# Kernel optimization log

Measured on AMD Instinct MI355X. Metric: run time of the kernel, lower is better.

## Reference

```python
import jax, jax.numpy as jnp
import numpy as np

N, M, B = 2048, 2048, 1
D, H, DQK, DV = 1024, 16, 64, 64
OFFSET = 0
PARAM_SCALE = 0.02  # keeps logits in a sane range (original uses plain randn)


def setup_inputs() -> dict:
    key = jax.random.key(0)
    ks = jax.random.split(key, 7)
    return {
        "x_q": jax.random.normal(ks[0], (N, B, D), jnp.float32),
        "x_kv": jax.random.normal(ks[1], (M, B, D), jnp.float32),
        "to_q": jax.random.normal(ks[2], (DQK, H, D), jnp.float32) * PARAM_SCALE,
        "to_k": jax.random.normal(ks[3], (DQK, H, D), jnp.float32) * PARAM_SCALE,
        "to_v": jax.random.normal(ks[4], (DV, H, D), jnp.float32) * PARAM_SCALE,
        "to_out": jax.random.normal(ks[5], (D, DV, H), jnp.float32) * PARAM_SCALE,
        "for_pos_enc": jax.random.normal(ks[6], (DQK, H, D), jnp.float32) * PARAM_SCALE,
    }


def _sincos(n, m, offset, d_x_kv, dtype):
    # relative distances i - j + offset range over [offset-(m-1), offset+(n-1)]
    r = jnp.arange(offset - (m - 1), offset + (n - 1) + 1, dtype=dtype)  # [R], R=n+m-1
    inv_freq = 1.0 / (10000.0 ** (jnp.arange(0.0, d_x_kv, 2.0, dtype=dtype) / d_x_kv))
    phases = r[:, None] * inv_freq[None, :]  # [R, d/2]
    return jnp.concatenate([jnp.sin(phases), jnp.cos(phases)], axis=-1)  # [R, d]


def reference(x_q, x_kv, to_q, to_k, to_v, to_out, for_pos_enc):
    n, b, _ = x_q.shape
    m = x_kv.shape[0]
    # q: [n, d_qk, b, h]
    q = jnp.einsum('dhb,nab->ndah', to_q, x_q)
    # content logits: [n, m, b, h]
    k = jnp.einsum('dhc,mac->mdah', to_k, x_kv)
    content = jnp.einsum('ndah,mdah->nmah', q, k)
    # relative positional encoding (same math as pos_enc[dists - min] then einsum,
    # but logits computed per relative position then gathered -> no [n,m,d,h] blowup)
    sincos = _sincos(n, m, OFFSET, x_kv.shape[-1], x_q.dtype)  # [R, d_x_kv]
    pe_rel = jnp.einsum('dhb,rb->rdh', for_pos_enc, sincos)    # [R, d_qk, h]
    pl_rel = jnp.einsum('ndah,rdh->nrah', q, pe_rel)            # [n, R, b, h]
    idx = jnp.arange(n)[:, None] - jnp.arange(m)[None, :] + (m - 1)  # dists - dists.min()
    position = pl_rel[jnp.arange(n)[:, None], idx]               # [n, m, b, h]
    logits = content + position
    # causal mask: True above diagonal shifted by 1+offset
    mask = jnp.triu(jnp.ones((n, m), bool), 1 + OFFSET)
    logits = jnp.where(mask[:, :, None, None], -jnp.inf, logits)
    weights = jax.nn.softmax(logits, axis=1)                     # softmax over m
    v = jnp.einsum('chb,mab->mach', to_v, x_kv)                  # [m, b, dv, h]
    ctx = jnp.einsum('nmah,mach->nach', weights, v)              # [n, b, dv, h]
    out = jnp.einsum('dch,nach->nad', to_out, ctx)               # [n, b, d]
    return out
```

## Files before the change

kernel.cpp:

```cpp
#include <hip/hip_runtime.h>
#include <hip/hip_bf16.h>

#define N_Q   2048
#define M_KV  2048
#define DIM   1024
#define NH    16
#define DHEAD 64
#define KDIM  1024
#define PEROWS 2112
#define PEBUF  2176

typedef __attribute__((ext_vector_type(8))) __bf16 bf16x8;
typedef __attribute__((ext_vector_type(4))) float  f32x4;

typedef __attribute__((address_space(1))) const unsigned char gbyte_t;
typedef __attribute__((address_space(3))) unsigned char lbyte_t;

__device__ __forceinline__ unsigned short f2bf(float f) {
  union { float f; unsigned u; } v; v.f = f;
  unsigned u = v.u;
  u = u + 0x7fffu + ((u >> 16) & 1u);
  return (unsigned short)(u >> 16);
}

__global__ void cvt2_bf16_kernel(const float* __restrict__ xq, const float* __restrict__ xkv,
                                 unsigned short* __restrict__ oq, unsigned short* __restrict__ okv) {
  int e = blockIdx.x * 256 + threadIdx.x;
  if (e < N_Q * DIM) oq[e] = f2bf(xq[e]);
  else               okv[e - N_Q * DIM] = f2bf(xkv[e - N_Q * DIM]);
}

__global__ void pack4_kernel(const float* __restrict__ wq, const float* __restrict__ wk,
                             const float* __restrict__ wv, const float* __restrict__ wp,
                             unsigned short* __restrict__ oq, unsigned short* __restrict__ okv,
                             unsigned short* __restrict__ op) {
  int gid = blockIdx.x * 256 + threadIdx.x;
  int which = gid >> 20;
  int e = gid & ((1 << 20) - 1);
  int j = e >> 10, b = e & 1023;
  int d = j & 63, h = j >> 6;
  const float* w = (which == 0) ? wq : (which == 1) ? wk : (which == 2) ? wv : wp;
  unsigned short* o = (which == 0) ? oq : (which == 1) ? okv : (which == 2) ? (okv + (size_t)DIM * DIM) : op;
  o[e] = f2bf(w[(d * NH + h) * DIM + b]);
}

__global__ void pack_wo_kernel(const float* __restrict__ w,
                               unsigned short* __restrict__ out) {
  int e = blockIdx.x * 256 + threadIdx.x;
  int dd = e >> 10, j = e & 1023;
  int c = j & 63, h = j >> 6;
  out[e] = f2bf(w[(dd * DHEAD + c) * NH + h]);
}

__global__ void sincos_kernel(unsigned short* __restrict__ out) {
  int e = blockIdx.x * 256 + threadIdx.x;
  int r = e >> 10, i = e & 1023;
  int k2 = (i < 512) ? i : (i - 512);
  float ex = (float)(2 * k2) * (1.0f / 1024.0f);
  float invf = __expf(-ex * 9.210340371976184f);
  float ph = (float)(r - 63) * invf;
  out[e] = f2bf((i < 512) ? __sinf(ph) : __cosf(ph));
}

template<int MODE>
__global__ __launch_bounds__(256) void gemm128_kernel(
    const unsigned short* __restrict__ A, const unsigned short* __restrict__ B,
    void* __restrict__ C1, void* __restrict__ C2, int Mr, int maxBrow) {
  __shared__ unsigned short As[2][128][64];
  __shared__ unsigned short Bs[2][64][64];
  int tid  = threadIdx.x;
  int wave = tid >> 6, lane = tid & 63;
  int g = lane >> 4, r16 = lane & 15;
  int arow0 = blockIdx.x * 128;
  int brow0 = blockIdx.y * 64;
  int amax  = Mr - 1;

  auto stage = [&](int buf, int kt) {
    #pragma unroll
    for (int n = 0; n < 4; ++n) {
      int seg  = wave * 4 + n;
      int rloc = seg * 8 + (lane >> 3);
      int cbyte = ((lane & 7) << 4) ^ ((rloc & 7) << 4);
      int grow = min(arow0 + rloc, amax);
      const unsigned short* gp = A + (size_t)grow * KDIM + kt + (cbyte >> 1);
      __builtin_amdgcn_global_load_lds((gbyte_t*)(const void*)gp,
                                       (lbyte_t*)(void*)&As[buf][seg * 8][0], 16, 0, 0);
    }
    #pragma unroll
    for (int n = 0; n < 2; ++n) {
      int seg  = wave * 2 + n;
      int rloc = seg * 8 + (lane >> 3);
      int cbyte = ((lane & 7) << 4) ^ ((rloc & 7) << 4);
      int grow = min(brow0 + rloc, maxBrow);
      const unsigned short* gp = B + (size_t)grow * KDIM + kt + (cbyte >> 1);
      __builtin_amdgcn_global_load_lds((gbyte_t*)(const void*)gp,
                                       (lbyte_t*)(void*)&Bs[buf][seg * 8][0], 16, 0, 0);
    }
  };

  f32x4 acc[2][4];
  #pragma unroll
  for (int i = 0; i < 2; ++i)
    #pragma unroll
    for (int j = 0; j < 4; ++j) acc[i][j] = (f32x4){0,0,0,0};

  stage(0, 0);
  asm volatile("s_waitcnt vmcnt(0)" ::: "memory");
  __syncthreads();

  int buf = 0;
  for (int t = 0; t < 16; ++t) {
    if (t < 15) stage(buf ^ 1, (t + 1) * 64);

    bf16x8 af[2][2], bf[4][2];
    #pragma unroll
    for (int i = 0; i < 2; ++i)
      #pragma unroll
      for (int kk = 0; kk < 2; ++kk) {
        int r = wave * 32 + i * 16 + r16;
        int cb = ((kk << 6) | (g << 4)) ^ ((r & 7) << 4);
        af[i][kk] = *(const bf16x8*)((const char*)&As[buf][r][0] + cb);
      }
    #pragma unroll
    for (int j = 0; j < 4; ++j)
      #pragma unroll
      for (int kk = 0; kk < 2; ++kk) {
        int r = j * 16 + r16;
        int cb = ((kk << 6) | (g << 4)) ^ ((r & 7) << 4);
        bf[j][kk] = *(const bf16x8*)((const char*)&Bs[buf][r][0] + cb);
      }
    #pragma unroll
    for (int kk = 0; kk < 2; ++kk)
      #pragma unroll
      for (int i = 0; i < 2; ++i)
        #pragma unroll
        for (int j = 0; j < 4; ++j)
          acc[i][j] = __builtin_amdgcn_mfma_f32_16x16x32_bf16(af[i][kk], bf[j][kk], acc[i][j], 0, 0, 0);

    if (t < 15) {
      asm volatile("s_waitcnt vmcnt(0)" ::: "memory");
      __syncthreads();
      buf ^= 1;
    }
  }

  #pragma unroll
  for (int i = 0; i < 2; ++i)
    #pragma unroll
    for (int j = 0; j < 4; ++j)
      #pragma unroll
      for (int rr = 0; rr < 4; ++rr) {
        int row = arow0 + wave * 32 + i * 16 + g * 4 + rr;
        int col = brow0 + j * 16 + r16;
        float v = acc[i][j][rr];
        if (MODE == 0) {
          if (row < Mr) ((float*)C1)[(size_t)row * 1024 + col] = v;
        } else if (MODE == 1) {
          if (row < Mr) ((unsigned short*)C1)[(size_t)row * 1024 + col] = f2bf(v);
        } else {
          if (col < 1024) ((unsigned short*)C1)[(size_t)row * 1024 + col] = f2bf(v);
          else            ((unsigned short*)C2)[(size_t)(col - 1024) * M_KV + row] = f2bf(v);
        }
      }
}

__global__ __launch_bounds__(256, 2) void attn_mfma_kernel(
    const unsigned short* __restrict__ qb, const unsigned short* __restrict__ kb,
    const unsigned short* __restrict__ vt, const unsigned short* __restrict__ pe,
    unsigned short* __restrict__ ctx, float* __restrict__ part) {
  int ord  = (int)blockIdx.x;
  int h    = ord & 15;
  int widx = 79 - (ord >> 4);
  int b, c;
  if (widx < 8)       { b = widx;                                  c = 0; }
  else if (widx < 24) { int t2 = widx - 8;  b = 8  + (t2 >> 1);    c = t2 & 1; }
  else if (widx < 48) { int t2 = widx - 24; int q3 = t2 / 3; b = 16 + q3; c = t2 - 3 * q3; }
  else                { int t2 = widx - 48; b = 24 + (t2 >> 2);    c = t2 & 3; }
  int n0   = b * 64;
  int nc   = (b < 8) ? 1 : (b >> 3) + 1;
  int t0   = c * 8;
  int tend = min(t0 + 8, b + 1);

  int wave = threadIdx.x >> 6;
  int lane = threadIdx.x & 63;
  int g    = lane >> 4;
  int r16  = lane & 15;

  __shared__ unsigned short Ks[2][64][64];
  __shared__ unsigned short Vs[2][64][64];
  __shared__ unsigned short PEs[2][128][64];
  __shared__ unsigned short W_lds[4][16][72];

  const unsigned short* qrow = qb + (size_t)(n0 + wave * 16 + r16) * DIM + h * 64 + g * 8;
  bf16x8 aq0 = *(const bf16x8*)(qrow);
  bf16x8 aq1 = *(const bf16x8*)(qrow + 32);

  union { unsigned short u[8]; bf16x8 v; } one_u;
  #pragma unroll
  for (int i = 0; i < 8; ++i) one_u.u[i] = 0x3F80;
  bf16x8 ones = one_u.v;

  f32x4 acc[4] = {{0,0,0,0},{0,0,0,0},{0,0,0,0},{0,0,0,0}};
  f32x4 lacc = {0,0,0,0};

  auto stage = [&](int bufn, int tilen) {
    int m0n = tilen * 64;
    int prb = n0 - m0n;
    #pragma unroll
    for (int n = 0; n < 2; ++n) {
      int seg  = wave * 2 + n;
      int rloc = seg * 8 + (lane >> 3);
      int cbyte = ((lane & 7) << 4) ^ ((rloc & 7) << 4);
      const unsigned short* gpk = kb + (size_t)(m0n + rloc) * KDIM + h * 64 + (cbyte >> 1);
      __builtin_amdgcn_global_load_lds((gbyte_t*)(const void*)gpk,
                                       (lbyte_t*)(void*)&Ks[bufn][seg * 8][0], 16, 0, 0);
      const unsigned short* gpv = vt + (size_t)(h * 64 + rloc) * M_KV + m0n + (cbyte >> 1);
      __builtin_amdgcn_global_load_lds((gbyte_t*)(const void*)gpv,
                                       (lbyte_t*)(void*)&Vs[bufn][seg * 8][0], 16, 0, 0);
    }
    #pragma unroll
    for (int n = 0; n < 4; ++n) {
      int seg  = wave * 4 + n;
      int rloc = seg * 8 + (lane >> 3);
      int cbyte = ((lane & 7) << 4) ^ ((rloc & 7) << 4);
      const unsigned short* gpp = pe + (size_t)(prb + rloc) * KDIM + h * 64 + (cbyte >> 1);
      __builtin_amdgcn_global_load_lds((gbyte_t*)(const void*)gpp,
                                       (lbyte_t*)(void*)&PEs[bufn][seg * 8][0], 16, 0, 0);
    }
  };

  int srcl[4]; bool hi_sel[4];
  #pragma unroll
  for (int rr = 0; rr < 4; ++rr) {
    srcl[rr]   = (g << 4) | ((g * 4 + rr + 63 - r16) & 15);
    hi_sel[rr] = (g * 4 + rr) > r16;
  }
  int sw = (r16 & 7) << 4;

  stage(0, t0);
  asm volatile("s_waitcnt vmcnt(0)" ::: "memory");
  __syncthreads();

  int buf = 0;
  for (int tile = t0; tile < tend; ++tile) {
    int m0 = tile * 64;
    if (tile + 1 < tend) stage(buf ^ 1, tile + 1);

    f32x4 s[4];
    #pragma unroll
    for (int ct = 0; ct < 4; ++ct) {
      const char* kbase = (const char*)&Ks[buf][ct * 16 + r16][0];
      bf16x8 k0 = *(const bf16x8*)(kbase + (((g << 4)) ^ sw));
      bf16x8 k1 = *(const bf16x8*)(kbase + ((64 | (g << 4)) ^ sw));
      f32x4 z = {0,0,0,0};
      z = __builtin_amdgcn_mfma_f32_16x16x32_bf16(aq0, k0, z, 0, 0, 0);
      z = __builtin_amdgcn_mfma_f32_16x16x32_bf16(aq1, k1, z, 0, 0, 0);
      s[ct] = z;
    }

    f32x4 z2[5];
    #pragma unroll
    for (int cp = 0; cp < 5; ++cp) {
      const char* pbase = (const char*)&PEs[buf][wave * 16 + cp * 16 + r16][0];
      bf16x8 p0 = *(const bf16x8*)(pbase + (((g << 4)) ^ sw));
      bf16x8 p1 = *(const bf16x8*)(pbase + ((64 | (g << 4)) ^ sw));
      f32x4 z = {0,0,0,0};
      z = __builtin_amdgcn_mfma_f32_16x16x32_bf16(aq0, p0, z, 0, 0, 0);
      z = __builtin_amdgcn_mfma_f32_16x16x32_bf16(aq1, p1, z, 0, 0, 0);
      z2[cp] = z;
    }

    bool diag = (m0 == n0);
    #pragma unroll
    for (int ct = 0; ct < 4; ++ct) {
      #pragma unroll
      for (int rr = 0; rr < 4; ++rr) {
        float vhi = __shfl(z2[4 - ct][rr], srcl[rr], 64);
        float vlo = __shfl(z2[3 - ct][rr], srcl[rr], 64);
        float p   = hi_sel[rr] ? vhi : vlo;
        int il = g * 4 + rr;
        int it = wave * 16 + il;
        int jt = ct * 16 + r16;
        float val = s[ct][rr] + p;
        if (diag && jt > it) val = -1e30f;
        s[ct][rr] = __expf(val);
      }
    }

    #pragma unroll
    for (int ct = 0; ct < 4; ++ct)
      #pragma unroll
      for (int rr = 0; rr < 4; ++rr)
        W_lds[wave][g * 4 + rr][ct * 16 + r16] = f2bf(s[ct][rr]);
    bf16x8 aw0 = *(const bf16x8*)(&W_lds[wave][r16][g * 8]);
    bf16x8 aw1 = *(const bf16x8*)(&W_lds[wave][r16][g * 8 + 32]);

    #pragma unroll
    for (int ct = 0; ct < 4; ++ct) {
      const char* vbase = (const char*)&Vs[buf][ct * 16 + r16][0];
      bf16x8 v0 = *(const bf16x8*)(vbase + (((g << 4)) ^ sw));
      bf16x8 v1 = *(const bf16x8*)(vbase + ((64 | (g << 4)) ^ sw));
      f32x4 a = acc[ct];
      a = __builtin_amdgcn_mfma_f32_16x16x32_bf16(aw0, v0, a, 0, 0, 0);
      a = __builtin_amdgcn_mfma_f32_16x16x32_bf16(aw1, v1, a, 0, 0, 0);
      acc[ct] = a;
    }
    lacc = __builtin_amdgcn_mfma_f32_16x16x32_bf16(aw0, ones, lacc, 0, 0, 0);
    lacc = __builtin_amdgcn_mfma_f32_16x16x32_bf16(aw1, ones, lacc, 0, 0, 0);

    asm volatile("s_waitcnt vmcnt(0)" ::: "memory");
    __syncthreads();
    buf ^= 1;
  }

  if (nc == 1) {
    #pragma unroll
    for (int rr = 0; rr < 4; ++rr) {
      float inv = 1.0f / lacc[rr];
      #pragma unroll
      for (int ct = 0; ct < 4; ++ct) {
        int row = n0 + wave * 16 + g * 4 + rr;
        ctx[(size_t)row * DIM + h * 64 + ct * 16 + r16] = f2bf(acc[ct][rr] * inv);
      }
    }
  } else {
    float* slot = part + ((size_t)((b - 8) * 16 + h) * 4 + c) * (64 * 68);
    #pragma unroll
    for (int ct = 0; ct < 4; ++ct)
      #pragma unroll
      for (int rr = 0; rr < 4; ++rr) {
        int row = wave * 16 + g * 4 + rr;
        slot[row * 68 + ct * 16 + r16] = acc[ct][rr];
      }
    if (r16 == 0) {
      #pragma unroll
      for (int rr = 0; rr < 4; ++rr) {
        int row = wave * 16 + g * 4 + rr;
        slot[row * 68 + 64] = lacc[rr];
      }
    }
  }
}

__global__ __launch_bounds__(256) void combine_kernel(const float* __restrict__ part,
                                                      unsigned short* __restrict__ ctx) {
  int bb = blockIdx.x;
  int h  = blockIdx.y;
  int b  = bb + 8;
  int nc = (b >> 3) + 1;
  int t  = threadIdx.x;
  int row = t >> 2, q = t & 3;
  const float* base = part + ((size_t)(bb * 16 + h) * 4) * (64 * 68) + row * 68;
  float lstar = 0.0f;
  for (int c2 = 0; c2 < nc; ++c2) lstar += base[c2 * 4352 + 64];
  float inv = 1.0f / lstar;
  for (int cc = 0; cc < 16; ++cc) {
    int col = q * 16 + cc;
    float o = 0.0f;
    for (int c2 = 0; c2 < nc; ++c2) o += base[c2 * 4352 + col];
    ctx[(size_t)(b * 64 + row) * DIM + h * 64 + col] = f2bf(o * inv);
  }
}

extern "C" void kernel_launch(void* const* d_in, const int* in_sizes, int n_in,
                              void* d_out, int out_size, void* d_ws, size_t ws_size,
                              hipStream_t stream) {
  const float* x_q    = (const float*)d_in[0];
  const float* x_kv   = (const float*)d_in[1];
  const float* to_q   = (const float*)d_in[2];
  const float* to_k   = (const float*)d_in[3];
  const float* to_v   = (const float*)d_in[4];
  const float* to_out = (const float*)d_in[5];
  const float* to_pe  = (const float*)d_in[6];

  char* ws = (char*)d_ws;
  size_t off = 0;
  auto alloc = [&](size_t bytes) -> char* {
    char* p = ws + off;
    off += (bytes + 255) & ~(size_t)255;
    return p;
  };

  unsigned short* xq_bf  = (unsigned short*)alloc((size_t)N_Q  * DIM * 2);
  unsigned short* xkv_bf = (unsigned short*)alloc((size_t)M_KV * DIM * 2);
  unsigned short* wq_bf  = (unsigned short*)alloc((size_t)DIM * DIM * 2);
  unsigned short* wkv_bf = (unsigned short*)alloc((size_t)2 * DIM * DIM * 2);
  unsigned short* wp_bf  = (unsigned short*)alloc((size_t)DIM * DIM * 2);
  unsigned short* wo_bf  = (unsigned short*)alloc((size_t)DIM * DIM * 2);
  unsigned short* sc_bf  = (unsigned short*)alloc((size_t)PEBUF * DIM * 2);
  unsigned short* q_bf   = (unsigned short*)alloc((size_t)N_Q  * DIM * 2);
  unsigned short* k_bf   = (unsigned short*)alloc((size_t)M_KV * DIM * 2);
  unsigned short* vt_bf  = (unsigned short*)alloc((size_t)DIM * M_KV * 2);
  unsigned short* pe_bf  = (unsigned short*)alloc((size_t)PEBUF * DIM * 2);
  unsigned short* ctx_bf = (unsigned short*)alloc((size_t)N_Q * DIM * 2);
  float*          part   = (float*)alloc((size_t)24 * 16 * 4 * 64 * 68 * 4);

  cvt2_bf16_kernel<<<16384, 256, 0, stream>>>(x_q, x_kv, xq_bf, xkv_bf);
  pack4_kernel<<<16384, 256, 0, stream>>>(to_q, to_k, to_v, to_pe, wq_bf, wkv_bf, wp_bf);
  pack_wo_kernel<<<4096, 256, 0, stream>>>(to_out, wo_bf);
  sincos_kernel<<<8704, 256, 0, stream>>>(sc_bf);

  gemm128_kernel<1><<<dim3(16, 16), 256, 0, stream>>>(xq_bf,  wq_bf,  q_bf,  nullptr, N_Q,  DIM - 1);
  gemm128_kernel<3><<<dim3(16, 32), 256, 0, stream>>>(xkv_bf, wkv_bf, k_bf,  vt_bf,   M_KV, 2 * DIM - 1);
  gemm128_kernel<1><<<dim3(17, 16), 256, 0, stream>>>(sc_bf,  wp_bf,  pe_bf, nullptr, PEROWS, DIM - 1);

  attn_mfma_kernel<<<1280, 256, 0, stream>>>(q_bf, k_bf, vt_bf, pe_bf, ctx_bf, part);
  combine_kernel<<<dim3(24, NH), 256, 0, stream>>>(part, ctx_bf);

  gemm128_kernel<0><<<dim3(16, 16), 256, 0, stream>>>(ctx_bf, wo_bf, (float*)d_out, nullptr, N_Q, DIM - 1);
}
```

Measured before the change: 151.9 us.

## Merge prep kernels and input GEMMs into single launches, add MFMA priority hints

Four elementwise prep kernels become one vectorized prep kernel, with float4 loads and ushort4 stores plus a sincosf-based table. The three input-projection GEMMs are combined into one launch that picks its operands from the block index. The output GEMM gets its own specialized kernel without row clamping. s_setprio brackets around the MFMA sections in the GEMMs and the attention kernel try to favour matrix issue. The aim is to cut launch overhead and tail underutilization and improve memory efficiency, at the cost of more branching in the merged kernels.

```diff
diff --git a/kernel.cpp b/kernel.cpp
--- a/kernel.cpp
+++ b/kernel.cpp
@@ -23,56 +23,87 @@
   return (unsigned short)(u >> 16);
 }
 
-__global__ void cvt2_bf16_kernel(const float* __restrict__ xq, const float* __restrict__ xkv,
-                                 unsigned short* __restrict__ oq, unsigned short* __restrict__ okv) {
-  int e = blockIdx.x * 256 + threadIdx.x;
-  if (e < N_Q * DIM) oq[e] = f2bf(xq[e]);
-  else               okv[e - N_Q * DIM] = f2bf(xkv[e - N_Q * DIM]);
-}
-
-__global__ void pack4_kernel(const float* __restrict__ wq, const float* __restrict__ wk,
-                             const float* __restrict__ wv, const float* __restrict__ wp,
-                             unsigned short* __restrict__ oq, unsigned short* __restrict__ okv,
-                             unsigned short* __restrict__ op) {
+#define PREP_A 524288
+#define PREP_B 1048576
+#define PREP_C 2097152
+#define PREP_D 2359296
+#define PREP_E 2916352
+__global__ __launch_bounds__(256) void prep_kernel(
+    const float* __restrict__ x_q, const float* __restrict__ x_kv,
+    const float* __restrict__ to_q, const float* __restrict__ to_k,
+    const float* __restrict__ to_v, const float* __restrict__ to_pe,
+    const float* __restrict__ to_out,
+    unsigned short* __restrict__ xq_bf, unsigned short* __restrict__ xkv_bf,
+    unsigned short* __restrict__ wq_bf, unsigned short* __restrict__ wkv_bf,
+    unsigned short* __restrict__ wp_bf, unsigned short* __restrict__ wo_bf,
+    unsigned short* __restrict__ sc_bf) {
   int gid = blockIdx.x * 256 + threadIdx.x;
-  int which = gid >> 20;
-  int e = gid & ((1 << 20) - 1);
-  int j = e >> 10, b = e & 1023;
-  int d = j & 63, h = j >> 6;
-  const float* w = (which == 0) ? wq : (which == 1) ? wk : (which == 2) ? wv : wp;
-  unsigned short* o = (which == 0) ? oq : (which == 1) ? okv : (which == 2) ? (okv + (size_t)DIM * DIM) : op;
-  o[e] = f2bf(w[(d * NH + h) * DIM + b]);
-}
-
-__global__ void pack_wo_kernel(const float* __restrict__ w,
-                               unsigned short* __restrict__ out) {
-  int e = blockIdx.x * 256 + threadIdx.x;
-  int dd = e >> 10, j = e & 1023;
-  int c = j & 63, h = j >> 6;
-  out[e] = f2bf(w[(dd * DHEAD + c) * NH + h]);
-}
-
-__global__ void sincos_kernel(unsigned short* __restrict__ out) {
-  int e = blockIdx.x * 256 + threadIdx.x;
-  int r = e >> 10, i = e & 1023;
-  int k2 = (i < 512) ? i : (i - 512);
-  float ex = (float)(2 * k2) * (1.0f / 1024.0f);
-  float invf = __expf(-ex * 9.210340371976184f);
-  float ph = (float)(r - 63) * invf;
-  out[e] = f2bf((i < 512) ? __sinf(ph) : __cosf(ph));
-}
-
-template<int MODE>
-__global__ __launch_bounds__(256) void gemm128_kernel(
-    const unsigned short* __restrict__ A, const unsigned short* __restrict__ B,
-    void* __restrict__ C1, void* __restrict__ C2, int Mr, int maxBrow) {
+  if (gid < PREP_B) {
+    const float* src = (gid < PREP_A) ? x_q : x_kv;
+    unsigned short* dst = (gid < PREP_A) ? xq_bf : xkv_bf;
+    int e4 = (gid < PREP_A ? gid : gid - PREP_A) * 4;
+    float4 v = *(const float4*)(src + e4);
+    ushort4 o = { f2bf(v.x), f2bf(v.y), f2bf(v.z), f2bf(v.w) };
+    *(ushort4*)(dst + e4) = o;
+  } else if (gid < PREP_C) {
+    int e = gid - PREP_B;
+    int which = e >> 18, inner = e & 262143;
+    int e4 = inner * 4;
+    int j = e4 >> 10, b = e4 & 1023;
+    int d = j & 63, h = j >> 6;
+    const float* w = (which == 0) ? to_q : (which == 1) ? to_k : (which == 2) ? to_v : to_pe;
+    unsigned short* o = (which == 0) ? wq_bf : (which == 1) ? wkv_bf
+                       : (which == 2) ? (wkv_bf + (size_t)DIM * DIM) : wp_bf;
+    float4 v = *(const float4*)(w + (size_t)(d * NH + h) * DIM + b);
+    ushort4 u = { f2bf(v.x), f2bf(v.y), f2bf(v.z), f2bf(v.w) };
+    *(ushort4*)(o + e4) = u;
+  } else if (gid < PREP_D) {
+    int e4 = (gid - PREP_C) * 4;
+    int dd = e4 >> 10, jc = e4 & 1023;
+    int c = jc & 63, h = jc >> 6;
+    const float* base = to_out + (size_t)(dd * DHEAD + c) * NH + h;
+    ushort4 u = { f2bf(base[0]), f2bf(base[16]), f2bf(base[32]), f2bf(base[48]) };
+    *(ushort4*)(wo_bf + e4) = u;
+  } else if (gid < PREP_E) {
+    int e = gid - PREP_D;
+    int r = e >> 8, t8 = e & 255;
+    float ph0base = (float)(r - 63);
+    unsigned short ss[2], cc[2];
+    #pragma unroll
+    for (int i = 0; i < 2; ++i) {
+      int k2 = t8 * 2 + i;
+      float invf = __expf((float)k2 * (-9.210340371976184f / 512.0f));
+      float s, c;
+      __sincosf(ph0base * invf, &s, &c);
+      ss[i] = f2bf(s); cc[i] = f2bf(c);
+    }
+    unsigned short* row = sc_bf + (size_t)r * DIM;
+    *(unsigned int*)(row + t8 * 2)       = (unsigned)ss[0] | ((unsigned)ss[1] << 16);
+    *(unsigned int*)(row + t8 * 2 + 512) = (unsigned)cc[0] | ((unsigned)cc[1] << 16);
+  }
+}
+
+__global__ __launch_bounds__(256) void gemm_in_kernel(
+    const unsigned short* __restrict__ xq, const unsigned short* __restrict__ xkv,
+    const unsigned short* __restrict__ sc,
+    const unsigned short* __restrict__ wq, const unsigned short* __restrict__ wkv,
+    const unsigned short* __restrict__ wp,
+    unsigned short* __restrict__ qout, unsigned short* __restrict__ kout,
+    unsigned short* __restrict__ vtout, unsigned short* __restrict__ peout) {
+  int bid = blockIdx.x;
+  const unsigned short *A, *B; unsigned short *C1, *C2;
+  int Mr, maxBrow, mode, ax, by;
+  if (bid < 256)      { int t = bid;       ax = t & 15; by = t >> 4; A = xq;  B = wq;  C1 = qout;  C2 = nullptr; Mr = N_Q;    maxBrow = DIM - 1;     mode = 1; }
+  else if (bid < 768) { int t = bid - 256; ax = t & 15; by = t >> 4; A = xkv; B = wkv; C1 = kout;  C2 = vtout;   Mr = M_KV;   maxBrow = 2 * DIM - 1; mode = 3; }
+  else                { int t = bid - 768; ax = t % 17; by = t / 17; A = sc;  B = wp;  C1 = peout; C2 = nullptr; Mr = PEROWS; maxBrow = DIM - 1;     mode = 1; }
+
   __shared__ unsigned short As[2][128][64];
   __shared__ unsigned short Bs[2][64][64];
   int tid  = threadIdx.x;
   int wave = tid >> 6, lane = tid & 63;
   int g = lane >> 4, r16 = lane & 15;
-  int arow0 = blockIdx.x * 128;
-  int brow0 = blockIdx.y * 64;
+  int arow0 = ax * 128;
+  int brow0 = by * 64;
   int amax  = Mr - 1;
 
   auto stage = [&](int buf, int kt) {
@@ -112,7 +143,7 @@
   for (int t = 0; t < 16; ++t) {
     if (t < 15) stage(buf ^ 1, (t + 1) * 64);
 
-    bf16x8 af[2][2], bf[4][2];
+    bf16x8 af[2][2], bfr[4][2];
     #pragma unroll
     for (int i = 0; i < 2; ++i)
       #pragma unroll
@@ -127,15 +158,17 @@
       for (int kk = 0; kk < 2; ++kk) {
         int r = j * 16 + r16;
         int cb = ((kk << 6) | (g << 4)) ^ ((r & 7) << 4);
-        bf[j][kk] = *(const bf16x8*)((const char*)&Bs[buf][r][0] + cb);
-      }
+        bfr[j][kk] = *(const bf16x8*)((const char*)&Bs[buf][r][0] + cb);
+      }
+    __builtin_amdgcn_s_setprio(1);
     #pragma unroll
     for (int kk = 0; kk < 2; ++kk)
       #pragma unroll
       for (int i = 0; i < 2; ++i)
         #pragma unroll
         for (int j = 0; j < 4; ++j)
-          acc[i][j] = __builtin_amdgcn_mfma_f32_16x16x32_bf16(af[i][kk], bf[j][kk], acc[i][j], 0, 0, 0);
+          acc[i][j] = __builtin_amdgcn_mfma_f32_16x16x32_bf16(af[i][kk], bfr[j][kk], acc[i][j], 0, 0, 0);
+    __builtin_amdgcn_s_setprio(0);
 
     if (t < 15) {
       asm volatile("s_waitcnt vmcnt(0)" ::: "memory");
@@ -153,14 +186,102 @@
         int row = arow0 + wave * 32 + i * 16 + g * 4 + rr;
         int col = brow0 + j * 16 + r16;
         float v = acc[i][j][rr];
-        if (MODE == 0) {
-          if (row < Mr) ((float*)C1)[(size_t)row * 1024 + col] = v;
-        } else if (MODE == 1) {
-          if (row < Mr) ((unsigned short*)C1)[(size_t)row * 1024 + col] = f2bf(v);
+        if (mode == 1) {
+          if (row < Mr) C1[(size_t)row * 1024 + col] = f2bf(v);
         } else {
-          if (col < 1024) ((unsigned short*)C1)[(size_t)row * 1024 + col] = f2bf(v);
-          else            ((unsigned short*)C2)[(size_t)(col - 1024) * M_KV + row] = f2bf(v);
+          if (col < 1024) C1[(size_t)row * 1024 + col] = f2bf(v);
+          else            C2[(size_t)(col - 1024) * M_KV + row] = f2bf(v);
         }
+      }
+}
+
+__global__ __launch_bounds__(256) void gemm_out_kernel(
+    const unsigned short* __restrict__ A, const unsigned short* __restrict__ B,
+    float* __restrict__ C1) {
+  __shared__ unsigned short As[2][128][64];
+  __shared__ unsigned short Bs[2][64][64];
+  int tid  = threadIdx.x;
+  int wave = tid >> 6, lane = tid & 63;
+  int g = lane >> 4, r16 = lane & 15;
+  int arow0 = blockIdx.x * 128;
+  int brow0 = blockIdx.y * 64;
+
+  auto stage = [&](int buf, int kt) {
+    #pragma unroll
+    for (int n = 0; n < 4; ++n) {
+      int seg  = wave * 4 + n;
+      int rloc = seg * 8 + (lane >> 3);
+      int cbyte = ((lane & 7) << 4) ^ ((rloc & 7) << 4);
+      const unsigned short* gp = A + (size_t)(arow0 + rloc) * KDIM + kt + (cbyte >> 1);
+      __builtin_amdgcn_global_load_lds((gbyte_t*)(const void*)gp,
+                                       (lbyte_t*)(void*)&As[buf][seg * 8][0], 16, 0, 0);
+    }
+    #pragma unroll
+    for (int n = 0; n < 2; ++n) {
+      int seg  = wave * 2 + n;
+      int rloc = seg * 8 + (lane >> 3);
+      int cbyte = ((lane & 7) << 4) ^ ((rloc & 7) << 4);
+      const unsigned short* gp = B + (size_t)(brow0 + rloc) * KDIM + kt + (cbyte >> 1);
+      __builtin_amdgcn_global_load_lds((gbyte_t*)(const void*)gp,
+                                       (lbyte_t*)(void*)&Bs[buf][seg * 8][0], 16, 0, 0);
+    }
+  };
+
+  f32x4 acc[2][4];
+  #pragma unroll
+  for (int i = 0; i < 2; ++i)
+    #pragma unroll
+    for (int j = 0; j < 4; ++j) acc[i][j] = (f32x4){0,0,0,0};
+
+  stage(0, 0);
+  asm volatile("s_waitcnt vmcnt(0)" ::: "memory");
+  __syncthreads();
+
+  int buf = 0;
+  for (int t = 0; t < 16; ++t) {
+    if (t < 15) stage(buf ^ 1, (t + 1) * 64);
+    bf16x8 af[2][2], bfr[4][2];
+    #pragma unroll
+    for (int i = 0; i < 2; ++i)
+      #pragma unroll
+      for (int kk = 0; kk < 2; ++kk) {
+        int r = wave * 32 + i * 16 + r16;
+        int cb = ((kk << 6) | (g << 4)) ^ ((r & 7) << 4);
+        af[i][kk] = *(const bf16x8*)((const char*)&As[buf][r][0] + cb);
+      }
+    #pragma unroll
+    for (int j = 0; j < 4; ++j)
+      #pragma unroll
+      for (int kk = 0; kk < 2; ++kk) {
+        int r = j * 16 + r16;
+        int cb = ((kk << 6) | (g << 4)) ^ ((r & 7) << 4);
+        bfr[j][kk] = *(const bf16x8*)((const char*)&Bs[buf][r][0] + cb);
+      }
+    __builtin_amdgcn_s_setprio(1);
+    #pragma unroll
+    for (int kk = 0; kk < 2; ++kk)
+      #pragma unroll
+      for (int i = 0; i < 2; ++i)
+        #pragma unroll
+        for (int j = 0; j < 4; ++j)
+          acc[i][j] = __builtin_amdgcn_mfma_f32_16x16x32_bf16(af[i][kk], bfr[j][kk], acc[i][j], 0, 0, 0);
+    __builtin_amdgcn_s_setprio(0);
+    if (t < 15) {
+      asm volatile("s_waitcnt vmcnt(0)" ::: "memory");
+      __syncthreads();
+      buf ^= 1;
+    }
+  }
+
+  #pragma unroll
+  for (int i = 0; i < 2; ++i)
+    #pragma unroll
+    for (int j = 0; j < 4; ++j)
+      #pragma unroll
+      for (int rr = 0; rr < 4; ++rr) {
+        int row = arow0 + wave * 32 + i * 16 + g * 4 + rr;
+        int col = brow0 + j * 16 + r16;
+        C1[(size_t)row * 1024 + col] = acc[i][j][rr];
       }
 }
 
@@ -247,6 +368,7 @@
     if (tile + 1 < tend) stage(buf ^ 1, tile + 1);
 
     f32x4 s[4];
+    __builtin_amdgcn_s_setprio(1);
     #pragma unroll
     for (int ct = 0; ct < 4; ++ct) {
       const char* kbase = (const char*)&Ks[buf][ct * 16 + r16][0];
@@ -269,6 +391,7 @@
       z = __builtin_amdgcn_mfma_f32_16x16x32_bf16(aq1, p1, z, 0, 0, 0);
       z2[cp] = z;
     }
+    __builtin_amdgcn_s_setprio(0);
 
     bool diag = (m0 == n0);
     #pragma unroll
@@ -295,6 +418,7 @@
     bf16x8 aw0 = *(const bf16x8*)(&W_lds[wave][r16][g * 8]);
     bf16x8 aw1 = *(const bf16x8*)(&W_lds[wave][r16][g * 8 + 32]);
 
+    __builtin_amdgcn_s_setprio(1);
     #pragma unroll
     for (int ct = 0; ct < 4; ++ct) {
       const char* vbase = (const char*)&Vs[buf][ct * 16 + r16][0];
@@ -307,6 +431,7 @@
     }
     lacc = __builtin_amdgcn_mfma_f32_16x16x32_bf16(aw0, ones, lacc, 0, 0, 0);
     lacc = __builtin_amdgcn_mfma_f32_16x16x32_bf16(aw1, ones, lacc, 0, 0, 0);
+    __builtin_amdgcn_s_setprio(0);
 
     asm volatile("s_waitcnt vmcnt(0)" ::: "memory");
     __syncthreads();
@@ -395,17 +520,14 @@
   unsigned short* ctx_bf = (unsigned short*)alloc((size_t)N_Q * DIM * 2);
   float*          part   = (float*)alloc((size_t)24 * 16 * 4 * 64 * 68 * 4);
 
-  cvt2_bf16_kernel<<<16384, 256, 0, stream>>>(x_q, x_kv, xq_bf, xkv_bf);
-  pack4_kernel<<<16384, 256, 0, stream>>>(to_q, to_k, to_v, to_pe, wq_bf, wkv_bf, wp_bf);
-  pack_wo_kernel<<<4096, 256, 0, stream>>>(to_out, wo_bf);
-  sincos_kernel<<<8704, 256, 0, stream>>>(sc_bf);
-
-  gemm128_kernel<1><<<dim3(16, 16), 256, 0, stream>>>(xq_bf,  wq_bf,  q_bf,  nullptr, N_Q,  DIM - 1);
-  gemm128_kernel<3><<<dim3(16, 32), 256, 0, stream>>>(xkv_bf, wkv_bf, k_bf,  vt_bf,   M_KV, 2 * DIM - 1);
-  gemm128_kernel<1><<<dim3(17, 16), 256, 0, stream>>>(sc_bf,  wp_bf,  pe_bf, nullptr, PEROWS, DIM - 1);
+  prep_kernel<<<11392, 256, 0, stream>>>(x_q, x_kv, to_q, to_k, to_v, to_pe, to_out,
+                                         xq_bf, xkv_bf, wq_bf, wkv_bf, wp_bf, wo_bf, sc_bf);
+
+  gemm_in_kernel<<<1040, 256, 0, stream>>>(xq_bf, xkv_bf, sc_bf, wq_bf, wkv_bf, wp_bf,
+                                           q_bf, k_bf, vt_bf, pe_bf);
 
   attn_mfma_kernel<<<1280, 256, 0, stream>>>(q_bf, k_bf, vt_bf, pe_bf, ctx_bf, part);
   combine_kernel<<<dim3(24, NH), 256, 0, stream>>>(part, ctx_bf);
 
-  gemm128_kernel<0><<<dim3(16, 16), 256, 0, stream>>>(ctx_bf, wo_bf, (float*)d_out, nullptr, N_Q, DIM - 1);
-}
+  gemm_out_kernel<<<dim3(16, 16), 256, 0, stream>>>(ctx_bf, wo_bf, (float*)d_out);
+}
```

Result: faster. 130.3 us (-14.2%).
